# Optimization experiments

Measured on AMD Instinct MI355X. Metric: run time of the kernel, lower is better.

## Reference

```python
import jax, jax.numpy as jnp
import numpy as np

N = 100000
E = 1600000
D_IN = 64
D_OUT = 64


def setup_inputs() -> dict:
    key = jax.random.key(0)
    k1, k2, k3, k4 = jax.random.split(key, 4)
    x = jax.random.normal(k1, (N, D_IN), dtype=jnp.float32)
    edge_index = jax.random.randint(k2, (2, E), 0, N, dtype=jnp.int32)
    # nn.Linear(in, out): weight [out, in]; we store W as [in, out] for x @ W
    W = jax.random.normal(k3, (D_IN, D_OUT), dtype=jnp.float32) * (1.0 / np.sqrt(D_IN))
    b = jax.random.normal(k4, (D_OUT,), dtype=jnp.float32) * 0.01
    return {"x": x, "edge_index": edge_index, "W": W, "b": b}


def reference(x, edge_index, W, b):
    n = x.shape[0]
    src, tgt = edge_index[0], edge_index[1]
    # gather neighbor feats and scatter-add into source nodes: agg[src] += x[tgt]
    agg = jax.ops.segment_sum(x[tgt], src, num_segments=n)  # [N, D_in]
    # degree normalization: bincount(src) + eps
    counts = jax.ops.segment_sum(jnp.ones((src.shape[0],), dtype=x.dtype), src,
                                 num_segments=n) + 1e-6  # [N]
    agg = agg / counts[:, None]
    return agg @ W + b  # [N, D_out]
```

## Files before the change

kernel.cpp:

```cpp
#include <hip/hip_runtime.h>
#include <hip/hip_fp16.h>

#define D 64
#define NPB 64
#define LOGNPB 6
#define BCAPS 224
#define NSHARD 8
#define FCHUNK 8192
#define SORTCAP 1792

typedef int v4i __attribute__((ext_vector_type(4)));

__device__ __forceinline__ float bcast(float v, int k) {
    return __uint_as_float(__builtin_amdgcn_readlane(__float_as_uint(v), k));
}

__global__ __launch_bounds__(256) void partition_edges(
    const int* __restrict__ src, const int* __restrict__ tgt,
    int* __restrict__ gcur, int* __restrict__ part, int E, int nbuck)
{
    extern __shared__ int hist[];
    int tid = threadIdx.x;
    int xsh = blockIdx.x & (NSHARD - 1);
    int* mycur  = gcur + (size_t)xsh * nbuck;
    int* mypart = part + (size_t)xsh * nbuck * BCAPS;

    for (int i = tid; i < nbuck; i += 256) hist[i] = 0;
    __syncthreads();

    int base = blockIdx.x * FCHUNK;
    int end = base + FCHUNK < E ? base + FCHUNK : E;
    int nfull = (end - base) & ~7;

    for (int i = base + tid * 8; i + 8 <= end; i += 256 * 8) {
        v4i s0 = *(const v4i*)(src + i);
        v4i s1 = *(const v4i*)(src + i + 4);
        int ss[8] = {s0.x, s0.y, s0.z, s0.w, s1.x, s1.y, s1.z, s1.w};
        #pragma unroll
        for (int j = 0; j < 8; ++j)
            atomicAdd(&hist[ss[j] >> LOGNPB], 1);
    }
    for (int i = base + nfull + tid; i < end; i += 256)
        atomicAdd(&hist[src[i] >> LOGNPB], 1);
    __syncthreads();

    for (int bkt = tid; bkt < nbuck; bkt += 256) {
        int h = hist[bkt];
        hist[bkt] = h ? atomicAdd(&mycur[bkt], h) : 0;
    }
    __syncthreads();

    for (int i = base + tid * 8; i + 8 <= end; i += 256 * 8) {
        v4i s0 = *(const v4i*)(src + i);
        v4i s1 = *(const v4i*)(src + i + 4);
        v4i t0 = *(const v4i*)(tgt + i);
        v4i t1 = *(const v4i*)(tgt + i + 4);
        int ss[8] = {s0.x, s0.y, s0.z, s0.w, s1.x, s1.y, s1.z, s1.w};
        int tt[8] = {t0.x, t0.y, t0.z, t0.w, t1.x, t1.y, t1.z, t1.w};
        int pos[8], bk[8];
        #pragma unroll
        for (int j = 0; j < 8; ++j) {
            bk[j] = ss[j] >> LOGNPB;
            pos[j] = atomicAdd(&hist[bk[j]], 1);
        }
        #pragma unroll
        for (int j = 0; j < 8; ++j)
            if ((unsigned)pos[j] < BCAPS)
                mypart[(size_t)bk[j] * BCAPS + pos[j]] =
                    ((ss[j] & (NPB - 1)) << 20) | tt[j];
    }
    for (int i = base + nfull + tid; i < end; i += 256) {
        int s = src[i], t = tgt[i];
        int b = s >> LOGNPB;
        int p = atomicAdd(&hist[b], 1);
        if ((unsigned)p < BCAPS)
            mypart[(size_t)b * BCAPS + p] = ((s & (NPB - 1)) << 20) | t;
    }
}

__global__ __launch_bounds__(256) void gemm_y(
    const float* __restrict__ x, const float* __restrict__ W,
    __half* __restrict__ y, int N, int nwaves)
{
    int lane = threadIdx.x & 63;
    if (blockIdx.x == 0 && threadIdx.x < D)
        y[(size_t)N * D + threadIdx.x] = __float2half(0.0f);

    float wcol[D];
    #pragma unroll
    for (int k = 0; k < D; ++k)
        wcol[k] = W[k * D + lane];

    int gw = blockIdx.x * 4 + (threadIdx.x >> 6);
    for (int n = gw * 4; n < N; n += nwaves * 4) {
        int i1 = n + 1 < N ? n + 1 : N - 1;
        int i2 = n + 2 < N ? n + 2 : N - 1;
        int i3 = n + 3 < N ? n + 3 : N - 1;
        float x0 = x[(size_t)n  * D + lane];
        float x1 = x[(size_t)i1 * D + lane];
        float x2 = x[(size_t)i2 * D + lane];
        float x3 = x[(size_t)i3 * D + lane];

        float o0 = 0, o1 = 0, o2 = 0, o3 = 0;
        #pragma unroll
        for (int k = 0; k < D; ++k) {
            float w = wcol[k];
            o0 += bcast(x0, k) * w;
            o1 += bcast(x1, k) * w;
            o2 += bcast(x2, k) * w;
            o3 += bcast(x3, k) * w;
        }
        y[(size_t)n * D + lane] = __float2half(o0);
        if (n + 1 < N) y[(size_t)(n + 1) * D + lane] = __float2half(o1);
        if (n + 2 < N) y[(size_t)(n + 2) * D + lane] = __float2half(o2);
        if (n + 3 < N) y[(size_t)(n + 3) * D + lane] = __float2half(o3);
    }
}

__global__ __launch_bounds__(256) void bucket_gather(
    const __half* __restrict__ y, const int* __restrict__ gcur,
    const int* __restrict__ part, const float* __restrict__ bias_v,
    float* __restrict__ out, int N, int nbuck, int zrow)
{
    __shared__ int cnt_s[NPB];
    __shared__ int off_s[NPB];
    __shared__ int cur_s[NPB];
    __shared__ int segc[NSHARD];
    __shared__ __align__(16) int sortbuf[SORTCAP];
    int tid = threadIdx.x, wave = tid >> 6, lane = tid & 63;
    int bk = blockIdx.x;

    if (tid < NPB) cnt_s[tid] = 0;
    if (tid < NSHARD) {
        int c = gcur[(size_t)tid * nbuck + bk];
        segc[tid] = c > BCAPS ? BCAPS : c;
    }
    for (int i = tid; i < SORTCAP; i += 256) sortbuf[i] = zrow;
    __syncthreads();

    for (int sh = 0; sh < NSHARD; ++sh) {
        int c = segc[sh];
        const int* seg = part + ((size_t)sh * nbuck + bk) * BCAPS;
        for (int i = tid; i < c; i += 256)
            atomicAdd(&cnt_s[seg[i] >> 20], 1);
    }
    __syncthreads();

    if (wave == 0) {
        int v = cnt_s[lane];
        int r = (v + 7) & ~7;
        int s = r;
        #pragma unroll
        for (int d = 1; d < NPB; d <<= 1) {
            int t = __shfl_up(s, d);
            if (lane >= d) s += t;
        }
        off_s[lane] = s - r;
        cur_s[lane] = s - r;
    }
    __syncthreads();

    for (int sh = 0; sh < NSHARD; ++sh) {
        int c = segc[sh];
        const int* seg = part + ((size_t)sh * nbuck + bk) * BCAPS;
        for (int i = tid; i < c; i += 256) {
            int w = seg[i];
            int p = atomicAdd(&cur_s[w >> 20], 1);
            if (p < SORTCAP) sortbuf[p] = w & 0xFFFFF;
        }
    }
    __syncthreads();

    float bias = bias_v[lane];
    for (int r = wave; r < NPB; r += 4) {
        int n = (bk << LOGNPB) + r;
        if (n >= N) break;
        int dg = cnt_s[r];
        int rdeg = (dg + 7) & ~7;
        int start = off_s[r];

        float a0 = 0, a1 = 0, a2 = 0, a3 = 0, a4 = 0, a5 = 0, a6 = 0, a7 = 0;
        for (int i = start; i < start + rdeg; i += 8) {
            int4 q0 = *(const int4*)&sortbuf[i];
            int4 q1 = *(const int4*)&sortbuf[i + 4];
            a0 += __half2float(y[(size_t)q0.x * D + lane]);
            a1 += __half2float(y[(size_t)q0.y * D + lane]);
            a2 += __half2float(y[(size_t)q0.z * D + lane]);
            a3 += __half2float(y[(size_t)q0.w * D + lane]);
            a4 += __half2float(y[(size_t)q1.x * D + lane]);
            a5 += __half2float(y[(size_t)q1.y * D + lane]);
            a6 += __half2float(y[(size_t)q1.z * D + lane]);
            a7 += __half2float(y[(size_t)q1.w * D + lane]);
        }
        float scale = 1.0f / ((float)dg + 1e-6f);
        float a = ((a0 + a1) + (a2 + a3)) + ((a4 + a5) + (a6 + a7));
        __builtin_nontemporal_store(a * scale + bias, &out[(size_t)n * D + lane]);
    }
}

extern "C" void kernel_launch(void* const* d_in, const int* in_sizes, int n_in,
                              void* d_out, int out_size, void* d_ws, size_t ws_size,
                              hipStream_t stream) {
    const float* x  = (const float*)d_in[0];
    const int*   ei = (const int*)d_in[1];
    const float* W  = (const float*)d_in[2];
    const float* b  = (const float*)d_in[3];
    float* out = (float*)d_out;

    int N = in_sizes[0] / D;
    int E = in_sizes[1] / 2;
    const int* src = ei;
    const int* tgt = ei + E;

    int nbuck = (N + NPB - 1) >> LOGNPB;

    int* gcur = (int*)d_ws;
    int* part = gcur + (size_t)NSHARD * nbuck;
    __half* y = (__half*)(part + (size_t)NSHARD * nbuck * BCAPS);

    hipMemsetAsync(gcur, 0, (size_t)NSHARD * nbuck * sizeof(int), stream);

    int fb = (E + FCHUNK - 1) / FCHUNK;
    partition_edges<<<fb, 256, nbuck * sizeof(int), stream>>>(
        src, tgt, gcur, part, E, nbuck);

    const int gemm_blocks = 1024;
    gemm_y<<<gemm_blocks, 256, 0, stream>>>(x, W, y, N, gemm_blocks * 4);

    bucket_gather<<<nbuck, 256, 0, stream>>>(y, gcur, part, b, out, N, nbuck, N);
}
```

Before: 185.6 us.

## Fuse edge partition and GEMM into one launch; gather two rows per wave

Merges the edge partitioning kernel and the x@W GEMM into a single launch, with blocks split by index, so the two independent stages can run at the same time and one launch is saved. The GEMM blocks now also allocate the dynamic shared histogram, which they never use, and that could reduce occupancy. The gather loop now processes two destination rows per wave at once, interleaved, to raise memory-level parallelism. The cost is extra divergence when the two rows have different degrees, plus more register pressure.

```diff
diff --git a/kernel.cpp b/kernel.cpp
--- a/kernel.cpp
+++ b/kernel.cpp
@@ -15,105 +15,106 @@
     return __uint_as_float(__builtin_amdgcn_readlane(__float_as_uint(v), k));
 }
 
-__global__ __launch_bounds__(256) void partition_edges(
+__global__ __launch_bounds__(256, 2) void fused_partition_gemm(
     const int* __restrict__ src, const int* __restrict__ tgt,
-    int* __restrict__ gcur, int* __restrict__ part, int E, int nbuck)
+    int* __restrict__ gcur, int* __restrict__ part,
+    const float* __restrict__ x, const float* __restrict__ W,
+    __half* __restrict__ y,
+    int E, int nbuck, int fill_blocks, int N, int gemm_nwaves)
 {
     extern __shared__ int hist[];
     int tid = threadIdx.x;
-    int xsh = blockIdx.x & (NSHARD - 1);
-    int* mycur  = gcur + (size_t)xsh * nbuck;
-    int* mypart = part + (size_t)xsh * nbuck * BCAPS;
-
-    for (int i = tid; i < nbuck; i += 256) hist[i] = 0;
-    __syncthreads();
-
-    int base = blockIdx.x * FCHUNK;
-    int end = base + FCHUNK < E ? base + FCHUNK : E;
-    int nfull = (end - base) & ~7;
-
-    for (int i = base + tid * 8; i + 8 <= end; i += 256 * 8) {
-        v4i s0 = *(const v4i*)(src + i);
-        v4i s1 = *(const v4i*)(src + i + 4);
-        int ss[8] = {s0.x, s0.y, s0.z, s0.w, s1.x, s1.y, s1.z, s1.w};
+
+    if ((int)blockIdx.x < fill_blocks) {
+        int xsh = blockIdx.x & (NSHARD - 1);
+        int* mycur  = gcur + (size_t)xsh * nbuck;
+        int* mypart = part + (size_t)xsh * nbuck * BCAPS;
+
+        for (int i = tid; i < nbuck; i += 256) hist[i] = 0;
+        __syncthreads();
+
+        int base = blockIdx.x * FCHUNK;
+        int end = base + FCHUNK < E ? base + FCHUNK : E;
+        int nfull = (end - base) & ~7;
+
+        for (int i = base + tid * 8; i + 8 <= end; i += 256 * 8) {
+            v4i s0 = *(const v4i*)(src + i);
+            v4i s1 = *(const v4i*)(src + i + 4);
+            int ss[8] = {s0.x, s0.y, s0.z, s0.w, s1.x, s1.y, s1.z, s1.w};
+            #pragma unroll
+            for (int j = 0; j < 8; ++j)
+                atomicAdd(&hist[ss[j] >> LOGNPB], 1);
+        }
+        for (int i = base + nfull + tid; i < end; i += 256)
+            atomicAdd(&hist[src[i] >> LOGNPB], 1);
+        __syncthreads();
+
+        for (int bkt = tid; bkt < nbuck; bkt += 256) {
+            int h = hist[bkt];
+            hist[bkt] = h ? atomicAdd(&mycur[bkt], h) : 0;
+        }
+        __syncthreads();
+
+        for (int i = base + tid * 8; i + 8 <= end; i += 256 * 8) {
+            v4i s0 = *(const v4i*)(src + i);
+            v4i s1 = *(const v4i*)(src + i + 4);
+            v4i t0 = *(const v4i*)(tgt + i);
+            v4i t1 = *(const v4i*)(tgt + i + 4);
+            int ss[8] = {s0.x, s0.y, s0.z, s0.w, s1.x, s1.y, s1.z, s1.w};
+            int tt[8] = {t0.x, t0.y, t0.z, t0.w, t1.x, t1.y, t1.z, t1.w};
+            int pos[8], bk[8];
+            #pragma unroll
+            for (int j = 0; j < 8; ++j) {
+                bk[j] = ss[j] >> LOGNPB;
+                pos[j] = atomicAdd(&hist[bk[j]], 1);
+            }
+            #pragma unroll
+            for (int j = 0; j < 8; ++j)
+                if ((unsigned)pos[j] < BCAPS)
+                    mypart[(size_t)bk[j] * BCAPS + pos[j]] =
+                        ((ss[j] & (NPB - 1)) << 20) | tt[j];
+        }
+        for (int i = base + nfull + tid; i < end; i += 256) {
+            int s = src[i], t = tgt[i];
+            int b = s >> LOGNPB;
+            int p = atomicAdd(&hist[b], 1);
+            if ((unsigned)p < BCAPS)
+                mypart[(size_t)b * BCAPS + p] = ((s & (NPB - 1)) << 20) | t;
+        }
+    } else {
+        int lane = tid & 63;
+        if ((int)blockIdx.x == fill_blocks && tid < D)
+            y[(size_t)N * D + tid] = __float2half(0.0f);
+
+        float wcol[D];
         #pragma unroll
-        for (int j = 0; j < 8; ++j)
-            atomicAdd(&hist[ss[j] >> LOGNPB], 1);
-    }
-    for (int i = base + nfull + tid; i < end; i += 256)
-        atomicAdd(&hist[src[i] >> LOGNPB], 1);
-    __syncthreads();
-
-    for (int bkt = tid; bkt < nbuck; bkt += 256) {
-        int h = hist[bkt];
-        hist[bkt] = h ? atomicAdd(&mycur[bkt], h) : 0;
-    }
-    __syncthreads();
-
-    for (int i = base + tid * 8; i + 8 <= end; i += 256 * 8) {
-        v4i s0 = *(const v4i*)(src + i);
-        v4i s1 = *(const v4i*)(src + i + 4);
-        v4i t0 = *(const v4i*)(tgt + i);
-        v4i t1 = *(const v4i*)(tgt + i + 4);
-        int ss[8] = {s0.x, s0.y, s0.z, s0.w, s1.x, s1.y, s1.z, s1.w};
-        int tt[8] = {t0.x, t0.y, t0.z, t0.w, t1.x, t1.y, t1.z, t1.w};
-        int pos[8], bk[8];
-        #pragma unroll
-        for (int j = 0; j < 8; ++j) {
-            bk[j] = ss[j] >> LOGNPB;
-            pos[j] = atomicAdd(&hist[bk[j]], 1);
-        }
-        #pragma unroll
-        for (int j = 0; j < 8; ++j)
-            if ((unsigned)pos[j] < BCAPS)
-                mypart[(size_t)bk[j] * BCAPS + pos[j]] =
-                    ((ss[j] & (NPB - 1)) << 20) | tt[j];
-    }
-    for (int i = base + nfull + tid; i < end; i += 256) {
-        int s = src[i], t = tgt[i];
-        int b = s >> LOGNPB;
-        int p = atomicAdd(&hist[b], 1);
-        if ((unsigned)p < BCAPS)
-            mypart[(size_t)b * BCAPS + p] = ((s & (NPB - 1)) << 20) | t;
-    }
-}
-
-__global__ __launch_bounds__(256) void gemm_y(
-    const float* __restrict__ x, const float* __restrict__ W,
-    __half* __restrict__ y, int N, int nwaves)
-{
-    int lane = threadIdx.x & 63;
-    if (blockIdx.x == 0 && threadIdx.x < D)
-        y[(size_t)N * D + threadIdx.x] = __float2half(0.0f);
-
-    float wcol[D];
-    #pragma unroll
-    for (int k = 0; k < D; ++k)
-        wcol[k] = W[k * D + lane];
-
-    int gw = blockIdx.x * 4 + (threadIdx.x >> 6);
-    for (int n = gw * 4; n < N; n += nwaves * 4) {
-        int i1 = n + 1 < N ? n + 1 : N - 1;
-        int i2 = n + 2 < N ? n + 2 : N - 1;
-        int i3 = n + 3 < N ? n + 3 : N - 1;
-        float x0 = x[(size_t)n  * D + lane];
-        float x1 = x[(size_t)i1 * D + lane];
-        float x2 = x[(size_t)i2 * D + lane];
-        float x3 = x[(size_t)i3 * D + lane];
-
-        float o0 = 0, o1 = 0, o2 = 0, o3 = 0;
-        #pragma unroll
-        for (int k = 0; k < D; ++k) {
-            float w = wcol[k];
-            o0 += bcast(x0, k) * w;
-            o1 += bcast(x1, k) * w;
-            o2 += bcast(x2, k) * w;
-            o3 += bcast(x3, k) * w;
-        }
-        y[(size_t)n * D + lane] = __float2half(o0);
-        if (n + 1 < N) y[(size_t)(n + 1) * D + lane] = __float2half(o1);
-        if (n + 2 < N) y[(size_t)(n + 2) * D + lane] = __float2half(o2);
-        if (n + 3 < N) y[(size_t)(n + 3) * D + lane] = __float2half(o3);
+        for (int k = 0; k < D; ++k)
+            wcol[k] = W[k * D + lane];
+
+        int gw = ((int)blockIdx.x - fill_blocks) * 4 + (tid >> 6);
+        for (int n = gw * 4; n < N; n += gemm_nwaves * 4) {
+            int i1 = n + 1 < N ? n + 1 : N - 1;
+            int i2 = n + 2 < N ? n + 2 : N - 1;
+            int i3 = n + 3 < N ? n + 3 : N - 1;
+            float x0 = x[(size_t)n  * D + lane];
+            float x1 = x[(size_t)i1 * D + lane];
+            float x2 = x[(size_t)i2 * D + lane];
+            float x3 = x[(size_t)i3 * D + lane];
+
+            float o0 = 0, o1 = 0, o2 = 0, o3 = 0;
+            #pragma unroll
+            for (int k = 0; k < D; ++k) {
+                float w = wcol[k];
+                o0 += bcast(x0, k) * w;
+                o1 += bcast(x1, k) * w;
+                o2 += bcast(x2, k) * w;
+                o3 += bcast(x3, k) * w;
+            }
+            y[(size_t)n * D + lane] = __float2half(o0);
+            if (n + 1 < N) y[(size_t)(n + 1) * D + lane] = __float2half(o1);
+            if (n + 2 < N) y[(size_t)(n + 2) * D + lane] = __float2half(o2);
+            if (n + 3 < N) y[(size_t)(n + 3) * D + lane] = __float2half(o3);
+        }
     }
 }
 
@@ -172,29 +173,58 @@
     __syncthreads();
 
     float bias = bias_v[lane];
-    for (int r = wave; r < NPB; r += 4) {
-        int n = (bk << LOGNPB) + r;
-        if (n >= N) break;
-        int dg = cnt_s[r];
-        int rdeg = (dg + 7) & ~7;
-        int start = off_s[r];
+    #pragma unroll 1
+    for (int j = 0; j < NPB / 4; j += 2) {
+        int r0 = j * 4 + wave;
+        int r1 = (j + 1) * 4 + wave;
+        int n0 = (bk << LOGNPB) + r0;
+        int n1 = (bk << LOGNPB) + r1;
+        bool v0 = n0 < N, v1 = n1 < N;
+        int dg0 = v0 ? cnt_s[r0] : 0;
+        int dg1 = v1 ? cnt_s[r1] : 0;
+        int rd0 = (dg0 + 7) & ~7;
+        int rd1 = (dg1 + 7) & ~7;
+        int st0 = off_s[r0], st1 = off_s[r1];
 
         float a0 = 0, a1 = 0, a2 = 0, a3 = 0, a4 = 0, a5 = 0, a6 = 0, a7 = 0;
-        for (int i = start; i < start + rdeg; i += 8) {
-            int4 q0 = *(const int4*)&sortbuf[i];
-            int4 q1 = *(const int4*)&sortbuf[i + 4];
-            a0 += __half2float(y[(size_t)q0.x * D + lane]);
-            a1 += __half2float(y[(size_t)q0.y * D + lane]);
-            a2 += __half2float(y[(size_t)q0.z * D + lane]);
-            a3 += __half2float(y[(size_t)q0.w * D + lane]);
-            a4 += __half2float(y[(size_t)q1.x * D + lane]);
-            a5 += __half2float(y[(size_t)q1.y * D + lane]);
-            a6 += __half2float(y[(size_t)q1.z * D + lane]);
-            a7 += __half2float(y[(size_t)q1.w * D + lane]);
-        }
-        float scale = 1.0f / ((float)dg + 1e-6f);
-        float a = ((a0 + a1) + (a2 + a3)) + ((a4 + a5) + (a6 + a7));
-        __builtin_nontemporal_store(a * scale + bias, &out[(size_t)n * D + lane]);
+        float b0 = 0, b1 = 0, b2 = 0, b3 = 0, b4 = 0, b5 = 0, b6 = 0, b7 = 0;
+        int mx = rd0 > rd1 ? rd0 : rd1;
+        for (int i = 0; i < mx; i += 8) {
+            if (i < rd0) {
+                int4 q0 = *(const int4*)&sortbuf[st0 + i];
+                int4 q1 = *(const int4*)&sortbuf[st0 + i + 4];
+                a0 += __half2float(y[(size_t)q0.x * D + lane]);
+                a1 += __half2float(y[(size_t)q0.y * D + lane]);
+                a2 += __half2float(y[(size_t)q0.z * D + lane]);
+                a3 += __half2float(y[(size_t)q0.w * D + lane]);
+                a4 += __half2float(y[(size_t)q1.x * D + lane]);
+                a5 += __half2float(y[(size_t)q1.y * D + lane]);
+                a6 += __half2float(y[(size_t)q1.z * D + lane]);
+                a7 += __half2float(y[(size_t)q1.w * D + lane]);
+            }
+            if (i < rd1) {
+                int4 p0 = *(const int4*)&sortbuf[st1 + i];
+                int4 p1 = *(const int4*)&sortbuf[st1 + i + 4];
+                b0 += __half2float(y[(size_t)p0.x * D + lane]);
+                b1 += __half2float(y[(size_t)p0.y * D + lane]);
+                b2 += __half2float(y[(size_t)p0.z * D + lane]);
+                b3 += __half2float(y[(size_t)p0.w * D + lane]);
+                b4 += __half2float(y[(size_t)p1.x * D + lane]);
+                b5 += __half2float(y[(size_t)p1.y * D + lane]);
+                b6 += __half2float(y[(size_t)p1.z * D + lane]);
+                b7 += __half2float(y[(size_t)p1.w * D + lane]);
+            }
+        }
+        if (v0) {
+            float s0 = 1.0f / ((float)dg0 + 1e-6f);
+            float a = ((a0 + a1) + (a2 + a3)) + ((a4 + a5) + (a6 + a7));
+            __builtin_nontemporal_store(a * s0 + bias, &out[(size_t)n0 * D + lane]);
+        }
+        if (v1) {
+            float s1 = 1.0f / ((float)dg1 + 1e-6f);
+            float bsum = ((b0 + b1) + (b2 + b3)) + ((b4 + b5) + (b6 + b7));
+            __builtin_nontemporal_store(bsum * s1 + bias, &out[(size_t)n1 * D + lane]);
+        }
     }
 }
 
@@ -221,11 +251,9 @@
     hipMemsetAsync(gcur, 0, (size_t)NSHARD * nbuck * sizeof(int), stream);
 
     int fb = (E + FCHUNK - 1) / FCHUNK;
-    partition_edges<<<fb, 256, nbuck * sizeof(int), stream>>>(
-        src, tgt, gcur, part, E, nbuck);
-
     const int gemm_blocks = 1024;
-    gemm_y<<<gemm_blocks, 256, 0, stream>>>(x, W, y, N, gemm_blocks * 4);
+    fused_partition_gemm<<<fb + gemm_blocks, 256, nbuck * sizeof(int), stream>>>(
+        src, tgt, gcur, part, x, W, y, E, nbuck, fb, N, gemm_blocks * 4);
 
     bucket_gather<<<nbuck, 256, 0, stream>>>(y, gcur, part, b, out, N, nbuck, N);
 }
```

New measurement: 170.6 us. -8.1%, faster.

## Fuse partition, GEMM and gather into one cooperative persistent kernel

Applied to the files above, without the earlier changes.

Replaces the memset and three kernel launches with a single cooperative kernel that uses grid-wide syncs. After the first sync, the first fb blocks partition edges while the remaining blocks compute the fp16 projection at the same time. After the second sync, blocks loop persistently over the buckets to gather. The goal is to remove launch gaps and overlap partitioning with the GEMM. In exchange it adds grid.sync costs, caps the grid at occupancy times 256 CUs, and relies on a cached static grid size.

```diff
diff --git a/kernel.cpp b/kernel.cpp
--- a/kernel.cpp
+++ b/kernel.cpp
@@ -1,5 +1,8 @@
 #include <hip/hip_runtime.h>
 #include <hip/hip_fp16.h>
+#include <hip/hip_cooperative_groups.h>
+
+namespace cg = cooperative_groups;
 
 #define D 64
 #define NPB 64
@@ -15,186 +18,189 @@
     return __uint_as_float(__builtin_amdgcn_readlane(__float_as_uint(v), k));
 }
 
-__global__ __launch_bounds__(256) void partition_edges(
+__global__ __launch_bounds__(256, 4) void gcn_fused(
     const int* __restrict__ src, const int* __restrict__ tgt,
-    int* __restrict__ gcur, int* __restrict__ part, int E, int nbuck)
+    int* __restrict__ gcur, int* __restrict__ part,
+    const float* __restrict__ x, const float* __restrict__ W,
+    const float* __restrict__ bias_v, __half* __restrict__ y,
+    float* __restrict__ out, int E, int N, int nbuck, int fb)
 {
     extern __shared__ int hist[];
-    int tid = threadIdx.x;
-    int xsh = blockIdx.x & (NSHARD - 1);
-    int* mycur  = gcur + (size_t)xsh * nbuck;
-    int* mypart = part + (size_t)xsh * nbuck * BCAPS;
-
-    for (int i = tid; i < nbuck; i += 256) hist[i] = 0;
-    __syncthreads();
-
-    int base = blockIdx.x * FCHUNK;
-    int end = base + FCHUNK < E ? base + FCHUNK : E;
-    int nfull = (end - base) & ~7;
-
-    for (int i = base + tid * 8; i + 8 <= end; i += 256 * 8) {
-        v4i s0 = *(const v4i*)(src + i);
-        v4i s1 = *(const v4i*)(src + i + 4);
-        int ss[8] = {s0.x, s0.y, s0.z, s0.w, s1.x, s1.y, s1.z, s1.w};
-        #pragma unroll
-        for (int j = 0; j < 8; ++j)
-            atomicAdd(&hist[ss[j] >> LOGNPB], 1);
-    }
-    for (int i = base + nfull + tid; i < end; i += 256)
-        atomicAdd(&hist[src[i] >> LOGNPB], 1);
-    __syncthreads();
-
-    for (int bkt = tid; bkt < nbuck; bkt += 256) {
-        int h = hist[bkt];
-        hist[bkt] = h ? atomicAdd(&mycur[bkt], h) : 0;
-    }
-    __syncthreads();
-
-    for (int i = base + tid * 8; i + 8 <= end; i += 256 * 8) {
-        v4i s0 = *(const v4i*)(src + i);
-        v4i s1 = *(const v4i*)(src + i + 4);
-        v4i t0 = *(const v4i*)(tgt + i);
-        v4i t1 = *(const v4i*)(tgt + i + 4);
-        int ss[8] = {s0.x, s0.y, s0.z, s0.w, s1.x, s1.y, s1.z, s1.w};
-        int tt[8] = {t0.x, t0.y, t0.z, t0.w, t1.x, t1.y, t1.z, t1.w};
-        int pos[8], bk[8];
-        #pragma unroll
-        for (int j = 0; j < 8; ++j) {
-            bk[j] = ss[j] >> LOGNPB;
-            pos[j] = atomicAdd(&hist[bk[j]], 1);
-        }
-        #pragma unroll
-        for (int j = 0; j < 8; ++j)
-            if ((unsigned)pos[j] < BCAPS)
-                mypart[(size_t)bk[j] * BCAPS + pos[j]] =
-                    ((ss[j] & (NPB - 1)) << 20) | tt[j];
-    }
-    for (int i = base + nfull + tid; i < end; i += 256) {
-        int s = src[i], t = tgt[i];
-        int b = s >> LOGNPB;
-        int p = atomicAdd(&hist[b], 1);
-        if ((unsigned)p < BCAPS)
-            mypart[(size_t)b * BCAPS + p] = ((s & (NPB - 1)) << 20) | t;
-    }
-}
-
-__global__ __launch_bounds__(256) void gemm_y(
-    const float* __restrict__ x, const float* __restrict__ W,
-    __half* __restrict__ y, int N, int nwaves)
-{
-    int lane = threadIdx.x & 63;
-    if (blockIdx.x == 0 && threadIdx.x < D)
-        y[(size_t)N * D + threadIdx.x] = __float2half(0.0f);
-
-    float wcol[D];
-    #pragma unroll
-    for (int k = 0; k < D; ++k)
-        wcol[k] = W[k * D + lane];
-
-    int gw = blockIdx.x * 4 + (threadIdx.x >> 6);
-    for (int n = gw * 4; n < N; n += nwaves * 4) {
-        int i1 = n + 1 < N ? n + 1 : N - 1;
-        int i2 = n + 2 < N ? n + 2 : N - 1;
-        int i3 = n + 3 < N ? n + 3 : N - 1;
-        float x0 = x[(size_t)n  * D + lane];
-        float x1 = x[(size_t)i1 * D + lane];
-        float x2 = x[(size_t)i2 * D + lane];
-        float x3 = x[(size_t)i3 * D + lane];
-
-        float o0 = 0, o1 = 0, o2 = 0, o3 = 0;
-        #pragma unroll
-        for (int k = 0; k < D; ++k) {
-            float w = wcol[k];
-            o0 += bcast(x0, k) * w;
-            o1 += bcast(x1, k) * w;
-            o2 += bcast(x2, k) * w;
-            o3 += bcast(x3, k) * w;
-        }
-        y[(size_t)n * D + lane] = __float2half(o0);
-        if (n + 1 < N) y[(size_t)(n + 1) * D + lane] = __float2half(o1);
-        if (n + 2 < N) y[(size_t)(n + 2) * D + lane] = __float2half(o2);
-        if (n + 3 < N) y[(size_t)(n + 3) * D + lane] = __float2half(o3);
-    }
-}
-
-__global__ __launch_bounds__(256) void bucket_gather(
-    const __half* __restrict__ y, const int* __restrict__ gcur,
-    const int* __restrict__ part, const float* __restrict__ bias_v,
-    float* __restrict__ out, int N, int nbuck, int zrow)
-{
     __shared__ int cnt_s[NPB];
     __shared__ int off_s[NPB];
     __shared__ int cur_s[NPB];
     __shared__ int segc[NSHARD];
     __shared__ __align__(16) int sortbuf[SORTCAP];
+
+    cg::grid_group grid = cg::this_grid();
     int tid = threadIdx.x, wave = tid >> 6, lane = tid & 63;
-    int bk = blockIdx.x;
-
-    if (tid < NPB) cnt_s[tid] = 0;
-    if (tid < NSHARD) {
-        int c = gcur[(size_t)tid * nbuck + bk];
-        segc[tid] = c > BCAPS ? BCAPS : c;
+    int nblk = gridDim.x;
+
+    for (int i = blockIdx.x * 256 + tid; i < NSHARD * nbuck; i += nblk * 256)
+        gcur[i] = 0;
+    grid.sync();
+
+    if ((int)blockIdx.x < fb) {
+        int xsh = blockIdx.x & (NSHARD - 1);
+        int* mycur  = gcur + (size_t)xsh * nbuck;
+        int* mypart = part + (size_t)xsh * nbuck * BCAPS;
+
+        for (int i = tid; i < nbuck; i += 256) hist[i] = 0;
+        __syncthreads();
+
+        int base = blockIdx.x * FCHUNK;
+        int end = base + FCHUNK < E ? base + FCHUNK : E;
+        int nfull = (end - base) & ~7;
+
+        for (int i = base + tid * 8; i + 8 <= end; i += 256 * 8) {
+            v4i s0 = *(const v4i*)(src + i);
+            v4i s1 = *(const v4i*)(src + i + 4);
+            int ss[8] = {s0.x, s0.y, s0.z, s0.w, s1.x, s1.y, s1.z, s1.w};
+            #pragma unroll
+            for (int j = 0; j < 8; ++j)
+                atomicAdd(&hist[ss[j] >> LOGNPB], 1);
+        }
+        for (int i = base + nfull + tid; i < end; i += 256)
+            atomicAdd(&hist[src[i] >> LOGNPB], 1);
+        __syncthreads();
+
+        for (int bkt = tid; bkt < nbuck; bkt += 256) {
+            int h = hist[bkt];
+            hist[bkt] = h ? atomicAdd(&mycur[bkt], h) : 0;
+        }
+        __syncthreads();
+
+        for (int i = base + tid * 8; i + 8 <= end; i += 256 * 8) {
+            v4i s0 = *(const v4i*)(src + i);
+            v4i s1 = *(const v4i*)(src + i + 4);
+            v4i t0 = *(const v4i*)(tgt + i);
+            v4i t1 = *(const v4i*)(tgt + i + 4);
+            int ss[8] = {s0.x, s0.y, s0.z, s0.w, s1.x, s1.y, s1.z, s1.w};
+            int tt[8] = {t0.x, t0.y, t0.z, t0.w, t1.x, t1.y, t1.z, t1.w};
+            int pos[8], bk[8];
+            #pragma unroll
+            for (int j = 0; j < 8; ++j) {
+                bk[j] = ss[j] >> LOGNPB;
+                pos[j] = atomicAdd(&hist[bk[j]], 1);
+            }
+            #pragma unroll
+            for (int j = 0; j < 8; ++j)
+                if ((unsigned)pos[j] < BCAPS)
+                    mypart[(size_t)bk[j] * BCAPS + pos[j]] =
+                        ((ss[j] & (NPB - 1)) << 20) | tt[j];
+        }
+        for (int i = base + nfull + tid; i < end; i += 256) {
+            int s = src[i], t = tgt[i];
+            int b = s >> LOGNPB;
+            int p = atomicAdd(&hist[b], 1);
+            if ((unsigned)p < BCAPS)
+                mypart[(size_t)b * BCAPS + p] = ((s & (NPB - 1)) << 20) | t;
+        }
+    } else {
+        if ((int)blockIdx.x == fb && tid < D)
+            y[(size_t)N * D + tid] = __float2half(0.0f);
+
+        int gemm_nwaves = (nblk - fb) * 4;
+        float wcol[D];
+        #pragma unroll
+        for (int k = 0; k < D; ++k)
+            wcol[k] = W[k * D + lane];
+
+        int gw = ((int)blockIdx.x - fb) * 4 + wave;
+        for (int n = gw * 4; n < N; n += gemm_nwaves * 4) {
+            int i1 = n + 1 < N ? n + 1 : N - 1;
+            int i2 = n + 2 < N ? n + 2 : N - 1;
+            int i3 = n + 3 < N ? n + 3 : N - 1;
+            float x0 = x[(size_t)n  * D + lane];
+            float x1 = x[(size_t)i1 * D + lane];
+            float x2 = x[(size_t)i2 * D + lane];
+            float x3 = x[(size_t)i3 * D + lane];
+
+            float o0 = 0, o1 = 0, o2 = 0, o3 = 0;
+            #pragma unroll
+            for (int k = 0; k < D; ++k) {
+                float w = wcol[k];
+                o0 += bcast(x0, k) * w;
+                o1 += bcast(x1, k) * w;
+                o2 += bcast(x2, k) * w;
+                o3 += bcast(x3, k) * w;
+            }
+            y[(size_t)n * D + lane] = __float2half(o0);
+            if (n + 1 < N) y[(size_t)(n + 1) * D + lane] = __float2half(o1);
+            if (n + 2 < N) y[(size_t)(n + 2) * D + lane] = __float2half(o2);
+            if (n + 3 < N) y[(size_t)(n + 3) * D + lane] = __float2half(o3);
+        }
     }
-    for (int i = tid; i < SORTCAP; i += 256) sortbuf[i] = zrow;
-    __syncthreads();
-
-    for (int sh = 0; sh < NSHARD; ++sh) {
-        int c = segc[sh];
-        const int* seg = part + ((size_t)sh * nbuck + bk) * BCAPS;
-        for (int i = tid; i < c; i += 256)
-            atomicAdd(&cnt_s[seg[i] >> 20], 1);
-    }
-    __syncthreads();
-
-    if (wave == 0) {
-        int v = cnt_s[lane];
-        int r = (v + 7) & ~7;
-        int s = r;
-        #pragma unroll
-        for (int d = 1; d < NPB; d <<= 1) {
-            int t = __shfl_up(s, d);
-            if (lane >= d) s += t;
-        }
-        off_s[lane] = s - r;
-        cur_s[lane] = s - r;
-    }
-    __syncthreads();
-
-    for (int sh = 0; sh < NSHARD; ++sh) {
-        int c = segc[sh];
-        const int* seg = part + ((size_t)sh * nbuck + bk) * BCAPS;
-        for (int i = tid; i < c; i += 256) {
-            int w = seg[i];
-            int p = atomicAdd(&cur_s[w >> 20], 1);
-            if (p < SORTCAP) sortbuf[p] = w & 0xFFFFF;
-        }
-    }
-    __syncthreads();
+    grid.sync();
 
     float bias = bias_v[lane];
-    for (int r = wave; r < NPB; r += 4) {
-        int n = (bk << LOGNPB) + r;
-        if (n >= N) break;
-        int dg = cnt_s[r];
-        int rdeg = (dg + 7) & ~7;
-        int start = off_s[r];
-
-        float a0 = 0, a1 = 0, a2 = 0, a3 = 0, a4 = 0, a5 = 0, a6 = 0, a7 = 0;
-        for (int i = start; i < start + rdeg; i += 8) {
-            int4 q0 = *(const int4*)&sortbuf[i];
-            int4 q1 = *(const int4*)&sortbuf[i + 4];
-            a0 += __half2float(y[(size_t)q0.x * D + lane]);
-            a1 += __half2float(y[(size_t)q0.y * D + lane]);
-            a2 += __half2float(y[(size_t)q0.z * D + lane]);
-            a3 += __half2float(y[(size_t)q0.w * D + lane]);
-            a4 += __half2float(y[(size_t)q1.x * D + lane]);
-            a5 += __half2float(y[(size_t)q1.y * D + lane]);
-            a6 += __half2float(y[(size_t)q1.z * D + lane]);
-            a7 += __half2float(y[(size_t)q1.w * D + lane]);
-        }
-        float scale = 1.0f / ((float)dg + 1e-6f);
-        float a = ((a0 + a1) + (a2 + a3)) + ((a4 + a5) + (a6 + a7));
-        __builtin_nontemporal_store(a * scale + bias, &out[(size_t)n * D + lane]);
+    for (int bk = blockIdx.x; bk < nbuck; bk += nblk) {
+        __syncthreads();
+        if (tid < NPB) cnt_s[tid] = 0;
+        if (tid < NSHARD) {
+            int c = gcur[(size_t)tid * nbuck + bk];
+            segc[tid] = c > BCAPS ? BCAPS : c;
+        }
+        for (int i = tid; i < SORTCAP; i += 256) sortbuf[i] = N;
+        __syncthreads();
+
+        for (int sh = 0; sh < NSHARD; ++sh) {
+            int c = segc[sh];
+            const int* seg = part + ((size_t)sh * nbuck + bk) * BCAPS;
+            for (int i = tid; i < c; i += 256)
+                atomicAdd(&cnt_s[seg[i] >> 20], 1);
+        }
+        __syncthreads();
+
+        if (wave == 0) {
+            int v = cnt_s[lane];
+            int r = (v + 7) & ~7;
+            int s = r;
+            #pragma unroll
+            for (int d = 1; d < NPB; d <<= 1) {
+                int t = __shfl_up(s, d);
+                if (lane >= d) s += t;
+            }
+            off_s[lane] = s - r;
+            cur_s[lane] = s - r;
+        }
+        __syncthreads();
+
+        for (int sh = 0; sh < NSHARD; ++sh) {
+            int c = segc[sh];
+            const int* seg = part + ((size_t)sh * nbuck + bk) * BCAPS;
+            for (int i = tid; i < c; i += 256) {
+                int w = seg[i];
+                int p = atomicAdd(&cur_s[w >> 20], 1);
+                if (p < SORTCAP) sortbuf[p] = w & 0xFFFFF;
+            }
+        }
+        __syncthreads();
+
+        for (int r = wave; r < NPB; r += 4) {
+            int n = (bk << LOGNPB) + r;
+            if (n >= N) break;
+            int dg = cnt_s[r];
+            int rdeg = (dg + 7) & ~7;
+            int start = off_s[r];
+
+            float a0 = 0, a1 = 0, a2 = 0, a3 = 0, a4 = 0, a5 = 0, a6 = 0, a7 = 0;
+            for (int i = start; i < start + rdeg; i += 8) {
+                int4 q0 = *(const int4*)&sortbuf[i];
+                int4 q1 = *(const int4*)&sortbuf[i + 4];
+                a0 += __half2float(y[(size_t)q0.x * D + lane]);
+                a1 += __half2float(y[(size_t)q0.y * D + lane]);
+                a2 += __half2float(y[(size_t)q0.z * D + lane]);
+                a3 += __half2float(y[(size_t)q0.w * D + lane]);
+                a4 += __half2float(y[(size_t)q1.x * D + lane]);
+                a5 += __half2float(y[(size_t)q1.y * D + lane]);
+                a6 += __half2float(y[(size_t)q1.z * D + lane]);
+                a7 += __half2float(y[(size_t)q1.w * D + lane]);
+            }
+            float scale = 1.0f / ((float)dg + 1e-6f);
+            float a = ((a0 + a1) + (a2 + a3)) + ((a4 + a5) + (a6 + a7));
+            __builtin_nontemporal_store(a * scale + bias, &out[(size_t)n * D + lane]);
+        }
     }
 }
 
@@ -218,14 +224,21 @@
     int* part = gcur + (size_t)NSHARD * nbuck;
     __half* y = (__half*)(part + (size_t)NSHARD * nbuck * BCAPS);
 
-    hipMemsetAsync(gcur, 0, (size_t)NSHARD * nbuck * sizeof(int), stream);
-
     int fb = (E + FCHUNK - 1) / FCHUNK;
-    partition_edges<<<fb, 256, nbuck * sizeof(int), stream>>>(
-        src, tgt, gcur, part, E, nbuck);
-
-    const int gemm_blocks = 1024;
-    gemm_y<<<gemm_blocks, 256, 0, stream>>>(x, W, y, N, gemm_blocks * 4);
-
-    bucket_gather<<<nbuck, 256, 0, stream>>>(y, gcur, part, b, out, N, nbuck, N);
+    unsigned int shmem = (unsigned int)(nbuck * sizeof(int));
+
+    static int coop_grid = 0;
+    if (coop_grid == 0) {
+        int k = 0;
+        hipOccupancyMaxActiveBlocksPerMultiprocessor(&k, gcn_fused, 256, shmem);
+        if (k < 1) k = 1;
+        if (k > 8) k = 8;
+        coop_grid = k * 256;
+    }
+
+    void* args[] = {(void*)&src, (void*)&tgt, (void*)&gcur, (void*)&part,
+                    (void*)&x, (void*)&W, (void*)&b, (void*)&y, (void*)&out,
+                    (void*)&E, (void*)&N, (void*)&nbuck, (void*)&fb};
+    hipLaunchCooperativeKernel((const void*)gcn_fused, dim3(coop_grid),
+                               dim3(256), args, shmem, stream);
 }
```

After: 331.8 us. 78.7% more time.

## Fuse edge partition and GEMM into one launch, halve bucket node count

Applied to the files above, without the earlier changes.

Merges the edge partition kernel and the x@W GEMM kernel into a single launch whose blocks branch by index, so the two independent stages can run concurrently and one launch is saved. Bucket size drops from 64 to 32 nodes with smaller per-shard capacity, giving twice as many gather blocks with less work each. The gather's segment loops are rewritten so each half of the block handles one shard at a time. The risks are capacity overflow with smaller BCAPS/SORTCAP under skewed degree, a larger dynamic LDS histogram for every block, and GEMM blocks now also reserving that LDS.

```diff
diff --git a/kernel.cpp b/kernel.cpp
--- a/kernel.cpp
+++ b/kernel.cpp
@@ -2,12 +2,12 @@
 #include <hip/hip_fp16.h>
 
 #define D 64
-#define NPB 64
-#define LOGNPB 6
-#define BCAPS 224
+#define NPB 32
+#define LOGNPB 5
+#define BCAPS 128
 #define NSHARD 8
 #define FCHUNK 8192
-#define SORTCAP 1792
+#define SORTCAP 1024
 
 typedef int v4i __attribute__((ext_vector_type(4)));
 
@@ -15,105 +15,106 @@
     return __uint_as_float(__builtin_amdgcn_readlane(__float_as_uint(v), k));
 }
 
-__global__ __launch_bounds__(256) void partition_edges(
+__global__ __launch_bounds__(256, 2) void fused_partition_gemm(
     const int* __restrict__ src, const int* __restrict__ tgt,
-    int* __restrict__ gcur, int* __restrict__ part, int E, int nbuck)
+    int* __restrict__ gcur, int* __restrict__ part,
+    const float* __restrict__ x, const float* __restrict__ W,
+    __half* __restrict__ y,
+    int E, int nbuck, int fill_blocks, int N, int gemm_nwaves)
 {
     extern __shared__ int hist[];
     int tid = threadIdx.x;
-    int xsh = blockIdx.x & (NSHARD - 1);
-    int* mycur  = gcur + (size_t)xsh * nbuck;
-    int* mypart = part + (size_t)xsh * nbuck * BCAPS;
-
-    for (int i = tid; i < nbuck; i += 256) hist[i] = 0;
-    __syncthreads();
-
-    int base = blockIdx.x * FCHUNK;
-    int end = base + FCHUNK < E ? base + FCHUNK : E;
-    int nfull = (end - base) & ~7;
-
-    for (int i = base + tid * 8; i + 8 <= end; i += 256 * 8) {
-        v4i s0 = *(const v4i*)(src + i);
-        v4i s1 = *(const v4i*)(src + i + 4);
-        int ss[8] = {s0.x, s0.y, s0.z, s0.w, s1.x, s1.y, s1.z, s1.w};
+
+    if ((int)blockIdx.x < fill_blocks) {
+        int xsh = blockIdx.x & (NSHARD - 1);
+        int* mycur  = gcur + (size_t)xsh * nbuck;
+        int* mypart = part + (size_t)xsh * nbuck * BCAPS;
+
+        for (int i = tid; i < nbuck; i += 256) hist[i] = 0;
+        __syncthreads();
+
+        int base = blockIdx.x * FCHUNK;
+        int end = base + FCHUNK < E ? base + FCHUNK : E;
+        int nfull = (end - base) & ~7;
+
+        for (int i = base + tid * 8; i + 8 <= end; i += 256 * 8) {
+            v4i s0 = *(const v4i*)(src + i);
+            v4i s1 = *(const v4i*)(src + i + 4);
+            int ss[8] = {s0.x, s0.y, s0.z, s0.w, s1.x, s1.y, s1.z, s1.w};
+            #pragma unroll
+            for (int j = 0; j < 8; ++j)
+                atomicAdd(&hist[ss[j] >> LOGNPB], 1);
+        }
+        for (int i = base + nfull + tid; i < end; i += 256)
+            atomicAdd(&hist[src[i] >> LOGNPB], 1);
+        __syncthreads();
+
+        for (int bkt = tid; bkt < nbuck; bkt += 256) {
+            int h = hist[bkt];
+            hist[bkt] = h ? atomicAdd(&mycur[bkt], h) : 0;
+        }
+        __syncthreads();
+
+        for (int i = base + tid * 8; i + 8 <= end; i += 256 * 8) {
+            v4i s0 = *(const v4i*)(src + i);
+            v4i s1 = *(const v4i*)(src + i + 4);
+            v4i t0 = *(const v4i*)(tgt + i);
+            v4i t1 = *(const v4i*)(tgt + i + 4);
+            int ss[8] = {s0.x, s0.y, s0.z, s0.w, s1.x, s1.y, s1.z, s1.w};
+            int tt[8] = {t0.x, t0.y, t0.z, t0.w, t1.x, t1.y, t1.z, t1.w};
+            int pos[8], bk[8];
+            #pragma unroll
+            for (int j = 0; j < 8; ++j) {
+                bk[j] = ss[j] >> LOGNPB;
+                pos[j] = atomicAdd(&hist[bk[j]], 1);
+            }
+            #pragma unroll
+            for (int j = 0; j < 8; ++j)
+                if ((unsigned)pos[j] < BCAPS)
+                    mypart[(size_t)bk[j] * BCAPS + pos[j]] =
+                        ((ss[j] & (NPB - 1)) << 20) | tt[j];
+        }
+        for (int i = base + nfull + tid; i < end; i += 256) {
+            int s = src[i], t = tgt[i];
+            int b = s >> LOGNPB;
+            int p = atomicAdd(&hist[b], 1);
+            if ((unsigned)p < BCAPS)
+                mypart[(size_t)b * BCAPS + p] = ((s & (NPB - 1)) << 20) | t;
+        }
+    } else {
+        int lane = tid & 63;
+        if ((int)blockIdx.x == fill_blocks && tid < D)
+            y[(size_t)N * D + tid] = __float2half(0.0f);
+
+        float wcol[D];
         #pragma unroll
-        for (int j = 0; j < 8; ++j)
-            atomicAdd(&hist[ss[j] >> LOGNPB], 1);
-    }
-    for (int i = base + nfull + tid; i < end; i += 256)
-        atomicAdd(&hist[src[i] >> LOGNPB], 1);
-    __syncthreads();
-
-    for (int bkt = tid; bkt < nbuck; bkt += 256) {
-        int h = hist[bkt];
-        hist[bkt] = h ? atomicAdd(&mycur[bkt], h) : 0;
-    }
-    __syncthreads();
-
-    for (int i = base + tid * 8; i + 8 <= end; i += 256 * 8) {
-        v4i s0 = *(const v4i*)(src + i);
-        v4i s1 = *(const v4i*)(src + i + 4);
-        v4i t0 = *(const v4i*)(tgt + i);
-        v4i t1 = *(const v4i*)(tgt + i + 4);
-        int ss[8] = {s0.x, s0.y, s0.z, s0.w, s1.x, s1.y, s1.z, s1.w};
-        int tt[8] = {t0.x, t0.y, t0.z, t0.w, t1.x, t1.y, t1.z, t1.w};
-        int pos[8], bk[8];
-        #pragma unroll
-        for (int j = 0; j < 8; ++j) {
-            bk[j] = ss[j] >> LOGNPB;
-            pos[j] = atomicAdd(&hist[bk[j]], 1);
-        }
-        #pragma unroll
-        for (int j = 0; j < 8; ++j)
-            if ((unsigned)pos[j] < BCAPS)
-                mypart[(size_t)bk[j] * BCAPS + pos[j]] =
-                    ((ss[j] & (NPB - 1)) << 20) | tt[j];
-    }
-    for (int i = base + nfull + tid; i < end; i += 256) {
-        int s = src[i], t = tgt[i];
-        int b = s >> LOGNPB;
-        int p = atomicAdd(&hist[b], 1);
-        if ((unsigned)p < BCAPS)
-            mypart[(size_t)b * BCAPS + p] = ((s & (NPB - 1)) << 20) | t;
-    }
-}
-
-__global__ __launch_bounds__(256) void gemm_y(
-    const float* __restrict__ x, const float* __restrict__ W,
-    __half* __restrict__ y, int N, int nwaves)
-{
-    int lane = threadIdx.x & 63;
-    if (blockIdx.x == 0 && threadIdx.x < D)
-        y[(size_t)N * D + threadIdx.x] = __float2half(0.0f);
-
-    float wcol[D];
-    #pragma unroll
-    for (int k = 0; k < D; ++k)
-        wcol[k] = W[k * D + lane];
-
-    int gw = blockIdx.x * 4 + (threadIdx.x >> 6);
-    for (int n = gw * 4; n < N; n += nwaves * 4) {
-        int i1 = n + 1 < N ? n + 1 : N - 1;
-        int i2 = n + 2 < N ? n + 2 : N - 1;
-        int i3 = n + 3 < N ? n + 3 : N - 1;
-        float x0 = x[(size_t)n  * D + lane];
-        float x1 = x[(size_t)i1 * D + lane];
-        float x2 = x[(size_t)i2 * D + lane];
-        float x3 = x[(size_t)i3 * D + lane];
-
-        float o0 = 0, o1 = 0, o2 = 0, o3 = 0;
-        #pragma unroll
-        for (int k = 0; k < D; ++k) {
-            float w = wcol[k];
-            o0 += bcast(x0, k) * w;
-            o1 += bcast(x1, k) * w;
-            o2 += bcast(x2, k) * w;
-            o3 += bcast(x3, k) * w;
-        }
-        y[(size_t)n * D + lane] = __float2half(o0);
-        if (n + 1 < N) y[(size_t)(n + 1) * D + lane] = __float2half(o1);
-        if (n + 2 < N) y[(size_t)(n + 2) * D + lane] = __float2half(o2);
-        if (n + 3 < N) y[(size_t)(n + 3) * D + lane] = __float2half(o3);
+        for (int k = 0; k < D; ++k)
+            wcol[k] = W[k * D + lane];
+
+        int gw = ((int)blockIdx.x - fill_blocks) * 4 + (tid >> 6);
+        for (int n = gw * 4; n < N; n += gemm_nwaves * 4) {
+            int i1 = n + 1 < N ? n + 1 : N - 1;
+            int i2 = n + 2 < N ? n + 2 : N - 1;
+            int i3 = n + 3 < N ? n + 3 : N - 1;
+            float x0 = x[(size_t)n  * D + lane];
+            float x1 = x[(size_t)i1 * D + lane];
+            float x2 = x[(size_t)i2 * D + lane];
+            float x3 = x[(size_t)i3 * D + lane];
+
+            float o0 = 0, o1 = 0, o2 = 0, o3 = 0;
+            #pragma unroll
+            for (int k = 0; k < D; ++k) {
+                float w = wcol[k];
+                o0 += bcast(x0, k) * w;
+                o1 += bcast(x1, k) * w;
+                o2 += bcast(x2, k) * w;
+                o3 += bcast(x3, k) * w;
+            }
+            y[(size_t)n * D + lane] = __float2half(o0);
+            if (n + 1 < N) y[(size_t)(n + 1) * D + lane] = __float2half(o1);
+            if (n + 2 < N) y[(size_t)(n + 2) * D + lane] = __float2half(o2);
+            if (n + 3 < N) y[(size_t)(n + 3) * D + lane] = __float2half(o3);
+        }
     }
 }
 
@@ -138,33 +139,38 @@
     for (int i = tid; i < SORTCAP; i += 256) sortbuf[i] = zrow;
     __syncthreads();
 
-    for (int sh = 0; sh < NSHARD; ++sh) {
-        int c = segc[sh];
-        const int* seg = part + ((size_t)sh * nbuck + bk) * BCAPS;
-        for (int i = tid; i < c; i += 256)
-            atomicAdd(&cnt_s[seg[i] >> 20], 1);
+    int half = tid >> 7;
+    int hid  = tid & 127;
+
+    for (int sh = 0; sh < NSHARD; sh += 2) {
+        int c = segc[sh + half];
+        if (hid < c) {
+            int w = part[((size_t)(sh + half) * nbuck + bk) * BCAPS + hid];
+            atomicAdd(&cnt_s[w >> 20], 1);
+        }
     }
     __syncthreads();
 
     if (wave == 0) {
-        int v = cnt_s[lane];
+        int v = (lane < NPB) ? cnt_s[lane] : 0;
         int r = (v + 7) & ~7;
         int s = r;
         #pragma unroll
         for (int d = 1; d < NPB; d <<= 1) {
             int t = __shfl_up(s, d);
-            if (lane >= d) s += t;
-        }
-        off_s[lane] = s - r;
-        cur_s[lane] = s - r;
-    }
-    __syncthreads();
-
-    for (int sh = 0; sh < NSHARD; ++sh) {
-        int c = segc[sh];
-        const int* seg = part + ((size_t)sh * nbuck + bk) * BCAPS;
-        for (int i = tid; i < c; i += 256) {
-            int w = seg[i];
+            if ((lane & (NPB - 1)) >= d) s += t;
+        }
+        if (lane < NPB) {
+            off_s[lane] = s - r;
+            cur_s[lane] = s - r;
+        }
+    }
+    __syncthreads();
+
+    for (int sh = 0; sh < NSHARD; sh += 2) {
+        int c = segc[sh + half];
+        if (hid < c) {
+            int w = part[((size_t)(sh + half) * nbuck + bk) * BCAPS + hid];
             int p = atomicAdd(&cur_s[w >> 20], 1);
             if (p < SORTCAP) sortbuf[p] = w & 0xFFFFF;
         }
@@ -221,11 +227,9 @@
     hipMemsetAsync(gcur, 0, (size_t)NSHARD * nbuck * sizeof(int), stream);
 
     int fb = (E + FCHUNK - 1) / FCHUNK;
-    partition_edges<<<fb, 256, nbuck * sizeof(int), stream>>>(
-        src, tgt, gcur, part, E, nbuck);
-
     const int gemm_blocks = 1024;
-    gemm_y<<<gemm_blocks, 256, 0, stream>>>(x, W, y, N, gemm_blocks * 4);
+    fused_partition_gemm<<<fb + gemm_blocks, 256, nbuck * sizeof(int), stream>>>(
+        src, tgt, gcur, part, x, W, y, E, nbuck, fb, N, gemm_blocks * 4);
 
     bucket_gather<<<nbuck, 256, 0, stream>>>(y, gcur, part, b, out, N, nbuck, N);
 }
```

Measured after the change: 169.7 us. 8.6% less time.
